# Optimization experiments

Hardware: AMD Instinct MI355X
Metric: run time of the kernel (lower is better)

The kernel has to match this reference:

```python
import jax, jax.numpy as jnp
import numpy as np

S, E, H = 4096, 1024, 16
D = E // H
N_SEG = 64


def setup_inputs() -> dict:
    key = jax.random.key(0)
    ks = jax.random.split(key, 11)
    scale = 0.02
    inp = {
        "x": jax.random.normal(ks[0], (S, E), dtype=jnp.float32),
        "Wq": jax.random.normal(ks[1], (E, E), dtype=jnp.float32) * scale,
        "bq": jax.random.normal(ks[2], (E,), dtype=jnp.float32) * scale,
        "Wk": jax.random.normal(ks[3], (E, E), dtype=jnp.float32) * scale,
        "bk": jax.random.normal(ks[4], (E,), dtype=jnp.float32) * scale,
        "Wv": jax.random.normal(ks[5], (E, E), dtype=jnp.float32) * scale,
        "bv": jax.random.normal(ks[6], (E,), dtype=jnp.float32) * scale,
        "Wo": jax.random.normal(ks[7], (E, E), dtype=jnp.float32) * scale,
        "bo": jax.random.normal(ks[8], (E,), dtype=jnp.float32) * scale,
        "segment_ids": jnp.sort(jax.random.randint(ks[9], (S,), 0, N_SEG)).astype(jnp.int32),
        "pos": 100,
    }
    return inp


def reference(x, Wq, bq, Wk, bk, Wv, bv, Wo, bo, segment_ids, pos):
    # torch Linear: y = x @ W.T + b
    q = (x @ Wq.T + bq).reshape(S, H, D)  # [S, H, D]
    k = (x @ Wk.T + bk).reshape(S, H, D)
    v = (x @ Wv.T + bv).reshape(S, H, D)

    # same-segment mask (contiguous segments from gene-structure dividers)
    mask = segment_ids[:, None] == segment_ids[None, :]  # [S, S]

    # NOTE: original leaves out-of-segment scores at 0 (not -inf) and applies
    # softmax over the FULL row; also no 1/sqrt(d) scaling. Reproduce exactly.
    scores = jnp.einsum("shd,thd->hst", q, k)            # [H, S, S]
    scores = jnp.where(mask[None, :, :], scores, 0.0)
    weights = jax.nn.softmax(scores, axis=-1)            # softmax over full row

    wv = jnp.einsum("hst,thd->shd", weights, v).reshape(S, E)
    out = wv @ Wo.T + bo                                  # [S, E]

    # mean over the main context: tokens sharing pos's segment
    main = (segment_ids == segment_ids[pos]).astype(out.dtype)  # [S]
    result = (out * main[:, None]).sum(axis=0) / main.sum()
    return result
```

## Files before the change

kernel.cpp:

```cpp
#include <hip/hip_runtime.h>
#include <math.h>

#define SS 4096
#define EE 1024
#define HH 16
#define DD 64
#define RMAX 128
#define NCOL 128
#define NTR  8
#define NRED 8
#define NPROJ 1536
#define NBG 64
#define NVS 16
#define NATT 256

#define OFF_SUMX  64
#define OFF_BGA   1088
#define OFF_BETA  2112
#define OFF_ALPHA 3136
#define OFF_VSUM  3200
#define OFF_PART  8192
#define OFF_XT    (OFF_PART + EE * NCOL)
#define OFF_QH    (OFF_XT + EE * RMAX)
#define OFF_KTH   (OFF_QH + HH * RMAX * DD)
#define OFF_VH    (OFF_KTH + HH * DD * RMAX)

__device__ __forceinline__ void seg_scan(const int* __restrict__ seg,
                                         const int* __restrict__ posp,
                                         int* sh, int& s0, int& L) {
    if (threadIdx.x == 0) { sh[0] = SS; sh[1] = -1; }
    __syncthreads();
    int sid = seg[posp[0]];
    int lmin = SS, lmax = -1;
    for (int i = threadIdx.x; i < SS; i += 256)
        if (seg[i] == sid) { lmin = min(lmin, i); lmax = max(lmax, i); }
#pragma unroll
    for (int off = 32; off; off >>= 1) {
        lmin = min(lmin, __shfl_xor(lmin, off));
        lmax = max(lmax, __shfl_xor(lmax, off));
    }
    if ((threadIdx.x & 63) == 0) { atomicMin(&sh[0], lmin); atomicMax(&sh[1], lmax); }
    __syncthreads();
    s0 = sh[0];
    L  = sh[1] - sh[0] + 1;
    if (L > RMAX) L = RMAX;
    if (L < 1)    L = 1;
}

__global__ __launch_bounds__(256) void d0_kernel(
    const float* __restrict__ x, const int* __restrict__ seg,
    const int* __restrict__ posp, float* __restrict__ ws) {
    int bid = blockIdx.x, tid = threadIdx.x;
    if (bid < NCOL) {
        float* partT = ws + OFF_PART;
        int r0 = bid * (SS / NCOL);
        const float4* x4 = (const float4*)x;
        float4 a = make_float4(0.f, 0.f, 0.f, 0.f);
#pragma unroll 8
        for (int r = 0; r < SS / NCOL; ++r) {
            float4 v = x4[(size_t)(r0 + r) * 256 + tid];
            a.x += v.x; a.y += v.y; a.z += v.z; a.w += v.w;
        }
        partT[(size_t)(4 * tid + 0) * NCOL + bid] = a.x;
        partT[(size_t)(4 * tid + 1) * NCOL + bid] = a.y;
        partT[(size_t)(4 * tid + 2) * NCOL + bid] = a.z;
        partT[(size_t)(4 * tid + 3) * NCOL + bid] = a.w;
        return;
    }
    __shared__ float t[128 * 129];
    __shared__ int sh[2];
    int s0, L;
    seg_scan(seg, posp, sh, s0, L);
    int kb = bid - NCOL;
    if (kb == 0 && tid == 0) { ((int*)ws)[0] = s0; ((int*)ws)[1] = L; }
    int k0 = kb * 128;
    float* xT = ws + OFF_XT;
    for (int idx = tid; idx < 128 * 32; idx += 256) {
        int r = idx >> 5, c4 = idx & 31;
        float4 v = make_float4(0.f, 0.f, 0.f, 0.f);
        if (r < L) v = *(const float4*)(x + (size_t)(s0 + r) * EE + k0 + c4 * 4);
        t[r * 129 + c4 * 4 + 0] = v.x;
        t[r * 129 + c4 * 4 + 1] = v.y;
        t[r * 129 + c4 * 4 + 2] = v.z;
        t[r * 129 + c4 * 4 + 3] = v.w;
    }
    __syncthreads();
    for (int idx = tid; idx < 128 * 32; idx += 256) {
        int k = idx >> 5, r4 = idx & 31;
        float4 o;
        o.x = t[(r4 * 4 + 0) * 129 + k];
        o.y = t[(r4 * 4 + 1) * 129 + k];
        o.z = t[(r4 * 4 + 2) * 129 + k];
        o.w = t[(r4 * 4 + 3) * 129 + k];
        *(float4*)(xT + (size_t)(k0 + k) * RMAX + r4 * 4) = o;
    }
}

__global__ __launch_bounds__(256) void d1_kernel(
    const float* __restrict__ Wq, const float* __restrict__ bq,
    const float* __restrict__ Wk, const float* __restrict__ bk,
    const float* __restrict__ Wv, const float* __restrict__ bv,
    float* __restrict__ ws) {
    int bid = blockIdx.x, tid = threadIdx.x;
    if (bid < NRED) {
        if (bid == 0) {
            for (int i = tid; i < 1088; i += 256) (ws + OFF_BETA)[i] = 0.f;
        }
        const float* partT = ws + OFF_PART;
        int e  = bid * 128 + (tid >> 1);
        int c0 = (tid & 1) * 64;
        const float4* p4 = (const float4*)(partT + (size_t)e * NCOL + c0);
        float4 s4 = make_float4(0.f, 0.f, 0.f, 0.f);
#pragma unroll
        for (int i = 0; i < 16; ++i) {
            float4 v = p4[i];
            s4.x += v.x; s4.y += v.y; s4.z += v.z; s4.w += v.w;
        }
        float s = s4.x + s4.y + s4.z + s4.w;
        s += __shfl_xor(s, 1);
        if ((tid & 1) == 0) (ws + OFF_SUMX)[e] = s;
        return;
    }
    __shared__ float red[16 * 66];
    int L  = ((const int*)ws)[1];
    int Lp = (L + 63) & ~63;
    int pid = bid - NRED;
    int rt  = (pid >= 768) ? 1 : 0;
    int rem = pid - rt * 768;
    int m   = rem >> 8;
    int eb  = rem & 255;
    int r0  = rt * 64;
    if (r0 >= Lp) return;
    int e0 = eb * 4;
    const float* W = (m == 0) ? Wq : ((m == 1) ? Wk : Wv);
    const float* b = (m == 0) ? bq : ((m == 1) ? bk : bv);
    int lane = tid & 63;
    int w4 = __builtin_amdgcn_readfirstlane(tid >> 6);
    const float* xcol = ws + OFF_XT + r0 + lane;
    int kq = ((w4 + pid) & 3) * 256;
    int ko = ((pid >> 2) & 31) * 8;
    const float* wr0 = W + (size_t)e0 * EE + kq;
    float acc0 = 0.f, acc1 = 0.f, acc2 = 0.f, acc3 = 0.f;
    float xv0[8], xv1[8];
#pragma unroll
    for (int u = 0; u < 8; ++u) xv0[u] = xcol[(size_t)(kq + ko + u) * RMAX];
    for (int kk = 0; kk < 256; kk += 16) {
        int kA = (ko + kk) & 255;
        int kB = (ko + kk + 8) & 255;
        int kC = (ko + kk + 16) & 255;
#pragma unroll
        for (int u = 0; u < 8; ++u)
            xv1[u] = xcol[(size_t)(kq + kB + u) * RMAX];
#pragma unroll
        for (int u = 0; u < 8; ++u) {
            float w0 = wr0[0 * EE + kA + u];
            float w1 = wr0[1 * EE + kA + u];
            float w2 = wr0[2 * EE + kA + u];
            float w3 = wr0[3 * EE + kA + u];
            acc0 += xv0[u] * w0; acc1 += xv0[u] * w1;
            acc2 += xv0[u] * w2; acc3 += xv0[u] * w3;
        }
#pragma unroll
        for (int u = 0; u < 8; ++u)
            xv0[u] = xcol[(size_t)(kq + kC + u) * RMAX];
#pragma unroll
        for (int u = 0; u < 8; ++u) {
            float w0 = wr0[0 * EE + kB + u];
            float w1 = wr0[1 * EE + kB + u];
            float w2 = wr0[2 * EE + kB + u];
            float w3 = wr0[3 * EE + kB + u];
            acc0 += xv1[u] * w0; acc1 += xv1[u] * w1;
            acc2 += xv1[u] * w2; acc3 += xv1[u] * w3;
        }
    }
    red[(w4 * 4 + 0) * 66 + lane] = acc0;
    red[(w4 * 4 + 1) * 66 + lane] = acc1;
    red[(w4 * 4 + 2) * 66 + lane] = acc2;
    red[(w4 * 4 + 3) * 66 + lane] = acc3;
    __syncthreads();
    int p  = tid >> 6;
    int rg = r0 + lane;
    float* qh  = ws + OFF_QH;
    float* kTh = ws + OFF_KTH;
    float* vh  = ws + OFF_VH;
    int h = e0 >> 6, d0 = (e0 & 63) + p;
    float v = 0.f;
    if (rg < L)
        v = red[(0 * 4 + p) * 66 + lane] + red[(1 * 4 + p) * 66 + lane]
          + red[(2 * 4 + p) * 66 + lane] + red[(3 * 4 + p) * 66 + lane]
          + b[e0 + p];
    if (m == 1) kTh[(size_t)(h * DD + d0) * RMAX + rg] = v;
    else        ((m == 0) ? qh : vh)[((size_t)h * RMAX + rg) * DD + d0] = v;
}

__global__ __launch_bounds__(256) void d2_kernel(
    const float* __restrict__ Wv, const float* __restrict__ bv,
    float* __restrict__ ws) {
    __shared__ float qS[4 * 64];
    __shared__ float wS[4 * 128];
    __shared__ float vp_[4][64];
    const float* sumx = ws + OFF_SUMX;
    float* bgA    = ws + OFF_BGA;
    float* betap  = ws + OFF_BETA;
    float* alphap = ws + OFF_ALPHA;
    float* vsumh  = ws + OFF_VSUM;
    const float* qh  = ws + OFF_QH;
    const float* kTh = ws + OFF_KTH;
    const float* vh  = ws + OFF_VH;

    int bid = blockIdx.x, tid = threadIdx.x;
    int lane = tid & 63, wave = tid >> 6;
    int L  = ((const int*)ws)[1];
    int Lp = (L + 63) & ~63;

    if (bid < NBG) {
        int e = bid * 16 + (tid >> 4);
        int j = tid & 15;
        const float4* wr  = (const float4*)(Wv + (size_t)e * EE);
        const float4* sx4 = (const float4*)sumx;
        float p = 0.f;
#pragma unroll
        for (int jj = 0; jj < 16; ++jj) {
            float4 w = wr[jj * 16 + j], z = sx4[jj * 16 + j];
            p += w.x * z.x + w.y * z.y + w.z * z.z + w.w * z.w;
        }
        p += __shfl_xor(p, 8);
        p += __shfl_xor(p, 4);
        p += __shfl_xor(p, 2);
        p += __shfl_xor(p, 1);
        if (j == 0) bgA[e] = p + (float)SS * bv[e];
        return;
    }
    if (bid < NBG + NVS) {
        int h = bid - NBG;
        float s = 0.f;
        for (int t = wave; t < Lp; t += 4)
            s += vh[((size_t)h * RMAX + t) * DD + lane];
        vp_[wave][lane] = s;
        __syncthreads();
        if (wave == 0)
            vsumh[h * DD + lane] = vp_[0][lane] + vp_[1][lane]
                                 + vp_[2][lane] + vp_[3][lane];
        return;
    }

    int aid = bid - NBG - NVS;
    int gidbase = aid * 4 + wave;
    int pairs = L * HH;
    float* qSw = qS + wave * 64;
    float* wSw = wS + wave * 128;
    for (int wg = gidbase; wg < pairs; wg += NATT * 4) {
        int h = wg & (HH - 1);
        int r = wg >> 4;
        qSw[lane] = qh[((size_t)h * RMAX + r) * DD + lane];
        float s0 = 0.f, s1 = 0.f;
#pragma unroll
        for (int d = 0; d < 64; ++d) {
            float qd = qSw[d];
            const float* kr = kTh + (size_t)(h * DD + d) * RMAX;
            s0 += qd * kr[lane];
            s1 += qd * kr[64 + lane];
        }
        float v0 = (lane < L)      ? s0 : -3.0e38f;
        float v1 = (64 + lane < L) ? s1 : -3.0e38f;
        float m = fmaxf(0.f, fmaxf(v0, v1));
#pragma unroll
        for (int off = 32; off; off >>= 1) m = fmaxf(m, __shfl_xor(m, off));
        float w0 = (lane < L)      ? __expf(s0 - m) : 0.f;
        float w1 = (64 + lane < L) ? __expf(s1 - m) : 0.f;
        float Zl = w0 + w1;
#pragma unroll
        for (int off = 32; off; off >>= 1) Zl += __shfl_xor(Zl, off);
        float em = __expf(-m);
        float Z  = Zl + (float)(SS - L) * em;
        wSw[lane]      = w0;
        wSw[64 + lane] = w1;
        float acc = 0.f;
#pragma unroll 16
        for (int t = 0; t < Lp; ++t)
            acc += wSw[t] * vh[((size_t)h * RMAX + t) * DD + lane];
        float invZ = 1.0f / Z;
        atomicAdd(&betap[h * DD + lane], acc * invZ);
        if (lane == 0) atomicAdd(&alphap[h], em * invZ);
    }
}

__global__ __launch_bounds__(256) void d3_kernel(
    const float* __restrict__ Wo, const float* __restrict__ bo,
    const float* __restrict__ ws, float* __restrict__ out) {
    __shared__ float z[EE];
    int tid = threadIdx.x;
    int lane = tid & 63, wave = tid >> 6;
    int L = ((const int*)ws)[1];

    {
        int h = tid >> 4;
        float4 beta = ((const float4*)(ws + OFF_BETA))[tid];
        float  a    = (ws + OFF_ALPHA)[h];
        float4 g    = ((const float4*)(ws + OFF_BGA))[tid];
        float4 vs   = ((const float4*)(ws + OFF_VSUM))[tid];
        ((float4*)z)[tid] = make_float4(beta.x + a * (g.x - vs.x),
                                        beta.y + a * (g.y - vs.y),
                                        beta.z + a * (g.z - vs.z),
                                        beta.w + a * (g.w - vs.w));
    }
    __syncthreads();

    int e = blockIdx.x * 4 + wave;
    const float4* wr = (const float4*)(Wo + (size_t)e * EE);
    const float4* z4 = (const float4*)z;
    float p = 0.f;
#pragma unroll
    for (int it = 0; it < 4; ++it) {
        float4 w = wr[it * 64 + lane], zz = z4[it * 64 + lane];
        p += w.x * zz.x + w.y * zz.y + w.z * zz.z + w.w * zz.w;
    }
#pragma unroll
    for (int off = 32; off; off >>= 1) p += __shfl_xor(p, off);
    if (lane == 0) out[e] = bo[e] + p / (float)L;
}

extern "C" void kernel_launch(void* const* d_in, const int* in_sizes, int n_in,
                              void* d_out, int out_size, void* d_ws, size_t ws_size,
                              hipStream_t stream) {
    const float* x   = (const float*)d_in[0];
    const float* Wq  = (const float*)d_in[1];
    const float* bq  = (const float*)d_in[2];
    const float* Wk  = (const float*)d_in[3];
    const float* bk  = (const float*)d_in[4];
    const float* Wv  = (const float*)d_in[5];
    const float* bv  = (const float*)d_in[6];
    const float* Wo  = (const float*)d_in[7];
    const float* bo  = (const float*)d_in[8];
    const int*   seg = (const int*)d_in[9];
    const int*   pos = (const int*)d_in[10];
    float*       out = (float*)d_out;
    float*       ws  = (float*)d_ws;

    d0_kernel<<<NCOL + NTR, 256, 0, stream>>>(x, seg, pos, ws);
    d1_kernel<<<NRED + NPROJ, 256, 0, stream>>>(Wq, bq, Wk, bk, Wv, bv, ws);
    d2_kernel<<<NBG + NVS + NATT, 256, 0, stream>>>(Wv, bv, ws);
    d3_kernel<<<EE / 4, 256, 0, stream>>>(Wo, bo, ws, out);
}
```

Baseline: 66.28 us.

## Split QKV projection K-reduction across blocks with separate reduce kernel

The projection kernel now gives each block one K-quarter, with each wave covering a different 4-column output group. Previously each block's four waves split K for the same four columns and combined the results in shared memory. Partial sums go to a new workspace buffer, and a new small kernel adds the four K-chunks, applies the bias and scatters into the Q/K^T/V layouts. This drops the shared-memory reduction and barrier and changes the W access pattern so the 16 rows a block touches are contiguous. The cost is an extra kernel launch plus a write and re-read of the partial-sum buffer in global memory.

```diff
diff --git a/kernel.cpp b/kernel.cpp
--- a/kernel.cpp
+++ b/kernel.cpp
@@ -10,6 +10,7 @@
 #define NTR  8
 #define NRED 8
 #define NPROJ 1536
+#define NREDB 96
 #define NBG 64
 #define NVS 16
 #define NATT 256
@@ -24,6 +25,7 @@
 #define OFF_QH    (OFF_XT + EE * RMAX)
 #define OFF_KTH   (OFF_QH + HH * RMAX * DD)
 #define OFF_VH    (OFF_KTH + HH * DD * RMAX)
+#define OFF_YP    (OFF_VH + HH * RMAX * DD)
 
 __device__ __forceinline__ void seg_scan(const int* __restrict__ seg,
                                          const int* __restrict__ posp,
@@ -97,10 +99,8 @@
 }
 
 __global__ __launch_bounds__(256) void d1_kernel(
-    const float* __restrict__ Wq, const float* __restrict__ bq,
-    const float* __restrict__ Wk, const float* __restrict__ bk,
-    const float* __restrict__ Wv, const float* __restrict__ bv,
-    float* __restrict__ ws) {
+    const float* __restrict__ Wq, const float* __restrict__ Wk,
+    const float* __restrict__ Wv, float* __restrict__ ws) {
     int bid = blockIdx.x, tid = threadIdx.x;
     if (bid < NRED) {
         if (bid == 0) {
@@ -121,24 +121,24 @@
         if ((tid & 1) == 0) (ws + OFF_SUMX)[e] = s;
         return;
     }
-    __shared__ float red[16 * 66];
     int L  = ((const int*)ws)[1];
     int Lp = (L + 63) & ~63;
     int pid = bid - NRED;
     int rt  = (pid >= 768) ? 1 : 0;
     int rem = pid - rt * 768;
-    int m   = rem >> 8;
-    int eb  = rem & 255;
+    int kc  = rem & 3;
+    int rem2 = rem >> 2;
+    int m   = rem2 / 64;
+    int eb  = rem2 - m * 64;
     int r0  = rt * 64;
     if (r0 >= Lp) return;
-    int e0 = eb * 4;
     const float* W = (m == 0) ? Wq : ((m == 1) ? Wk : Wv);
-    const float* b = (m == 0) ? bq : ((m == 1) ? bk : bv);
     int lane = tid & 63;
     int w4 = __builtin_amdgcn_readfirstlane(tid >> 6);
+    int e0 = eb * 16 + w4 * 4;
     const float* xcol = ws + OFF_XT + r0 + lane;
-    int kq = ((w4 + pid) & 3) * 256;
-    int ko = ((pid >> 2) & 31) * 8;
+    int kq = kc * 256;
+    int ko = (rem2 & 31) * 8;
     const float* wr0 = W + (size_t)e0 * EE + kq;
     float acc0 = 0.f, acc1 = 0.f, acc2 = 0.f, acc3 = 0.f;
     float xv0[8], xv1[8];
@@ -173,24 +173,56 @@
             acc2 += xv1[u] * w2; acc3 += xv1[u] * w3;
         }
     }
-    red[(w4 * 4 + 0) * 66 + lane] = acc0;
-    red[(w4 * 4 + 1) * 66 + lane] = acc1;
-    red[(w4 * 4 + 2) * 66 + lane] = acc2;
-    red[(w4 * 4 + 3) * 66 + lane] = acc3;
-    __syncthreads();
-    int p  = tid >> 6;
+    float* yp = ws + OFF_YP + ((size_t)(kc * 3 + m) * EE) * RMAX;
     int rg = r0 + lane;
+    yp[(size_t)(e0 + 0) * RMAX + rg] = acc0;
+    yp[(size_t)(e0 + 1) * RMAX + rg] = acc1;
+    yp[(size_t)(e0 + 2) * RMAX + rg] = acc2;
+    yp[(size_t)(e0 + 3) * RMAX + rg] = acc3;
+}
+
+__global__ __launch_bounds__(256) void d1b_kernel(
+    const float* __restrict__ bq, const float* __restrict__ bk,
+    const float* __restrict__ bv, float* __restrict__ ws) {
+    int bid = blockIdx.x, tid = threadIdx.x;
+    int L = ((const int*)ws)[1];
+    int Lp = (L + 63) & ~63;
+    int m  = bid / 32;
+    int et = bid % 32;
+    const float* b = (m == 0) ? bq : ((m == 1) ? bk : bv);
     float* qh  = ws + OFF_QH;
     float* kTh = ws + OFF_KTH;
     float* vh  = ws + OFF_VH;
-    int h = e0 >> 6, d0 = (e0 & 63) + p;
-    float v = 0.f;
-    if (rg < L)
-        v = red[(0 * 4 + p) * 66 + lane] + red[(1 * 4 + p) * 66 + lane]
-          + red[(2 * 4 + p) * 66 + lane] + red[(3 * 4 + p) * 66 + lane]
-          + b[e0 + p];
-    if (m == 1) kTh[(size_t)(h * DD + d0) * RMAX + rg] = v;
-    else        ((m == 0) ? qh : vh)[((size_t)h * RMAX + rg) * DD + d0] = v;
+    const float* yp = ws + OFF_YP;
+    int r4 = (tid & 31) * 4;
+    int ee = tid >> 5;
+#pragma unroll
+    for (int ep = 0; ep < 4; ++ep) {
+        int e = et * 32 + ep * 8 + ee;
+        size_t base = (size_t)e * RMAX + r4;
+        float4 s = make_float4(0.f, 0.f, 0.f, 0.f);
+        if (r4 < Lp) {
+#pragma unroll
+            for (int kc = 0; kc < 4; ++kc) {
+                float4 v = *(const float4*)(yp + ((size_t)(kc * 3 + m) * EE) * RMAX + base);
+                s.x += v.x; s.y += v.y; s.z += v.z; s.w += v.w;
+            }
+        }
+        float bb = b[e];
+        float o[4] = {s.x + bb, s.y + bb, s.z + bb, s.w + bb};
+#pragma unroll
+        for (int i = 0; i < 4; ++i) if (r4 + i >= L) o[i] = 0.f;
+        int h = e >> 6, d = e & 63;
+        if (m == 1) {
+            *(float4*)(kTh + (size_t)(h * DD + d) * RMAX + r4) =
+                make_float4(o[0], o[1], o[2], o[3]);
+        } else {
+            float* y = (m == 0) ? qh : vh;
+#pragma unroll
+            for (int i = 0; i < 4; ++i)
+                y[((size_t)h * RMAX + r4 + i) * DD + d] = o[i];
+        }
+    }
 }
 
 __global__ __launch_bounds__(256) void d2_kernel(
@@ -338,7 +370,8 @@
     float*       ws  = (float*)d_ws;
 
     d0_kernel<<<NCOL + NTR, 256, 0, stream>>>(x, seg, pos, ws);
-    d1_kernel<<<NRED + NPROJ, 256, 0, stream>>>(Wq, bq, Wk, bk, Wv, bv, ws);
+    d1_kernel<<<NRED + NPROJ, 256, 0, stream>>>(Wq, Wk, Wv, ws);
+    d1b_kernel<<<NREDB, 256, 0, stream>>>(bq, bk, bv, ws);
     d2_kernel<<<NBG + NVS + NATT, 256, 0, stream>>>(Wv, bv, ws);
     d3_kernel<<<EE / 4, 256, 0, stream>>>(Wo, bo, ws, out);
 }
```

After: 77.09 us. 16.3% more time.
